# Performance work log

Measured on AMD Instinct MI355X. Metric: run time of the kernel, lower is better.

## Reference

```python
import jax, jax.numpy as jnp
import numpy as np

B, T, W = 4, 2048, 1024
K, G = 7, 8            # kernel_size, groups
Cg = W // G            # channels per group
SE_R = 16              # SE reduction ratio
LN_EPS = 1e-5


def setup_inputs() -> dict:
    key = jax.random.key(0)
    ks = jax.random.split(key, 8)
    h = jax.random.normal(ks[0], (B, T, W), jnp.float32)
    # mask: True = padding; valid prefix of random length per row
    lengths = jax.random.randint(ks[1], (B,), T // 2, T + 1)
    mask = jnp.arange(T)[None, :] >= lengths[:, None]
    s_w = np.float32(1.0 / np.sqrt(W))
    return dict(
        h=h,
        mask=mask,
        offset_w=jax.random.normal(ks[2], (W, K), jnp.float32) * 0.01,
        offset_b=jnp.zeros((K,), jnp.float32),
        conv_w=jax.random.normal(ks[3], (G, Cg, Cg, K), jnp.float32) * np.float32(1.0 / np.sqrt(Cg * K)),
        conv_b=jnp.zeros((W,), jnp.float32),
        ln_g=jnp.ones((W,), jnp.float32),
        ln_b=jnp.zeros((W,), jnp.float32),
        se_w1=jax.random.normal(ks[4], (W, W // SE_R), jnp.float32) * s_w,
        se_b1=jnp.zeros((W // SE_R,), jnp.float32),
        se_w2=jax.random.normal(ks[5], (W // SE_R, W), jnp.float32) * np.float32(1.0 / np.sqrt(W // SE_R)),
        se_b2=jnp.zeros((W,), jnp.float32),
        proj_w=jax.random.normal(ks[6], (W, 1), jnp.float32) * s_w,
        proj_b=jnp.zeros((1,), jnp.float32),
    )


def deform_conv1d(h, offset_w, offset_b, conv_w, conv_b):
    # h: [B,T,W]. Learned per-(position, tap) fractional offsets; linear interp gather;
    # grouped conv combine. conv_w: [G, out_per_group, in_per_group, K].
    Bn, Tn, Wn = h.shape
    pad = (K - 1) // 2
    offsets = h @ offset_w + offset_b                                   # [B,T,K]
    base = (jnp.arange(Tn, dtype=jnp.float32)[None, :, None]
            + (jnp.arange(K, dtype=jnp.float32) - pad)[None, None, :])  # [1,T,K]
    pos = jnp.clip(base + offsets, 0.0, Tn - 1.0)                       # [B,T,K]
    p0 = jnp.floor(pos).astype(jnp.int32)
    p1 = jnp.minimum(p0 + 1, Tn - 1)
    frac = (pos - p0.astype(jnp.float32))[..., None]                    # [B,T,K,1]
    gather = jax.vmap(lambda hb, ib: hb[ib])                            # [T,W],[T,K] -> [T,K,W]
    sampled = gather(h, p0) * (1.0 - frac) + gather(h, p1) * frac       # [B,T,K,W]
    sg = sampled.reshape(Bn, Tn, K, G, Cg)
    out = jnp.einsum('btkgc,gock->btgo', sg, conv_w).reshape(Bn, Tn, Wn)
    return out + conv_b


def layer_norm(x, g, b):
    mu = jnp.mean(x, axis=-1, keepdims=True)
    var = jnp.mean(jnp.square(x - mu), axis=-1, keepdims=True)
    return (x - mu) * jax.lax.rsqrt(var + LN_EPS) * g + b


def se_block(x, mask, w1, b1, w2, b2):
    valid = (~mask).astype(x.dtype)[..., None]                          # [B,T,1]
    lengths = jnp.clip(jnp.sum(valid, axis=1), 1.0)                     # [B,1]
    s = jnp.sum(x * valid, axis=1) / lengths                            # [B,W]
    gate = jax.nn.sigmoid(jax.nn.relu(s @ w1 + b1) @ w2 + b2)           # [B,W]
    return x * gate[:, None, :]


def reference(h, mask, offset_w, offset_b, conv_w, conv_b, ln_g, ln_b,
              se_w1, se_b1, se_w2, se_b2, proj_w, proj_b):
    x = layer_norm(deform_conv1d(h, offset_w, offset_b, conv_w, conv_b), ln_g, ln_b)
    x = se_block(x, mask, se_w1, se_b1, se_w2, se_b2)
    # dropout: identity in eval mode (p handled outside reference)
    valid = (~mask).astype(x.dtype)[..., None]
    x = x * valid                                                       # masked_fill(mask, 0)
    lengths = jnp.clip(jnp.sum(valid, axis=1), 1.0)                     # [B,1]
    pooled = jnp.sum(x, axis=1) / lengths                               # [B,W]
    return jnp.squeeze(pooled @ proj_w + proj_b, axis=-1)               # [B]
```

## Files before the change

### kernel.cpp

```cpp
#include <hip/hip_runtime.h>
#include <hip/hip_bf16.h>

#define Bdim 4
#define Tdim 2048
#define Wdim 1024
#define Kdim 7
#define Gdim 8
#define Cg   128
#define Hdim 64
#define TT   64

typedef __attribute__((ext_vector_type(8))) short short8v;
typedef __attribute__((ext_vector_type(4))) float float4v;

__device__ __forceinline__ short f2bf(float x) {
    union { float f; unsigned u; } v; v.f = x;
    unsigned r = v.u + 0x7fff + ((v.u >> 16) & 1);
    return (short)(r >> 16);
}

__device__ __forceinline__ unsigned pack2bf(float lo, float hi) {
    return __builtin_amdgcn_perm(__float_as_uint(hi) + 0x8000u,
                                 __float_as_uint(lo) + 0x8000u, 0x07060302u);
}

__device__ __forceinline__ short8v lerp_pack(uint4 a, uint4 b, float f) {
    union { uint4 u; short8v s; } r;
    const unsigned* pa = (const unsigned*)&a;
    const unsigned* pb = (const unsigned*)&b;
    unsigned* pr = (unsigned*)&r.u;
#pragma unroll
    for (int d = 0; d < 4; d++) {
        float alo = __uint_as_float(pa[d] << 16);
        float ahi = __uint_as_float(pa[d] & 0xffff0000u);
        float blo = __uint_as_float(pb[d] << 16);
        float bhi = __uint_as_float(pb[d] & 0xffff0000u);
        float rlo = alo + f * (blo - alo);
        float rhi = ahi + f * (bhi - ahi);
        pr[d] = pack2bf(rlo, rhi);
    }
    return r.s;
}

__global__ __launch_bounds__(256) void k_pre(const float* __restrict__ conv_w,
                                             short* __restrict__ Wtb,
                                             const float* __restrict__ h,
                                             const float* __restrict__ offset_w,
                                             const float* __restrict__ offset_b,
                                             float* __restrict__ pos,
                                             ushort* __restrict__ h16,
                                             float* __restrict__ s_sum) {
    int tid = threadIdx.x;
    if (blockIdx.x < 448) {
        if (blockIdx.x == 0) {
#pragma unroll
            for (int i = 0; i < 16; i++) s_sum[tid + i * 256] = 0.f;
        }
        int i = blockIdx.x * 256 + tid;
        int cb = i & 15;
        int o = (i >> 4) & 127;
        int gk = i >> 11;
        int k = gk % Kdim, g = gk / Kdim;
        const float* src = conv_w + ((size_t)(g * Cg + o) * Cg + cb * 8) * Kdim + k;
        short8v pk;
#pragma unroll
        for (int j = 0; j < 8; j++) pk[j] = f2bf(src[(size_t)j * Kdim]);
        short8v* Wtb8 = (short8v*)Wtb;
        Wtb8[(size_t)gk * 2048 + o * 16 + cb] = pk;
        return;
    }
    int lane = tid & 63, wv = tid >> 6;
    int bt = (blockIdx.x - 448) * 4 + wv;
    int t = bt & (Tdim - 1);
    const float* row = h + (size_t)bt * Wdim;
    float acc[Kdim];
#pragma unroll
    for (int k = 0; k < Kdim; k++) acc[k] = 0.f;
#pragma unroll
    for (int j = 0; j < 4; j++) {
        int c = lane * 4 + j * 256;
        float4 hv = *(const float4*)(row + c);
        const float* ow = offset_w + (size_t)c * Kdim;
#pragma unroll
        for (int k = 0; k < Kdim; k++)
            acc[k] += hv.x * ow[k] + hv.y * ow[Kdim + k] + hv.z * ow[2 * Kdim + k]
                    + hv.w * ow[3 * Kdim + k];
        ushort4 hp;
        hp.x = (ushort)f2bf(hv.x); hp.y = (ushort)f2bf(hv.y);
        hp.z = (ushort)f2bf(hv.z); hp.w = (ushort)f2bf(hv.w);
        *(ushort4*)(h16 + (size_t)bt * Wdim + c) = hp;
    }
#pragma unroll
    for (int k = 0; k < Kdim; k++) {
#pragma unroll
        for (int m = 32; m > 0; m >>= 1) acc[k] += __shfl_xor(acc[k], m);
    }
    if (lane < Kdim) {
        float o = acc[lane] + offset_b[lane];
        float base = (float)t + (float)(lane - 3);
        float p = fminf(fmaxf(base + o, 0.f), (float)(Tdim - 1));
        pos[bt * Kdim + lane] = p;
    }
}

__global__ __launch_bounds__(256, 4) void k_conv(const ushort* __restrict__ h16,
                                                 const short* __restrict__ Wtb,
                                                 const float* __restrict__ conv_b,
                                                 const float* __restrict__ pos,
                                                 ushort* __restrict__ y16) {
    __shared__ short8v sA8[2][TT * 16];

    int blk = blockIdx.x;
    int g  = blk & 7;
    int tc = (blk >> 3) & 31;
    int b  = blk >> 8;
    int t0 = tc * TT;
    int tid = threadIdx.x;
    int lane = tid & 63, wv = tid >> 6;
    int r15 = lane & 15, q = lane >> 4;

    const ushort* hb = h16 + (size_t)(b * Tdim) * Wdim + g * Cg;
    const short8v* WtbV = (const short8v*)Wtb + (size_t)(g * Kdim) * 2048;

    int scb = tid & 15;
    int sr0 = tid >> 4;

    float4v acc[4][2];
#pragma unroll
    for (int tt = 0; tt < 4; tt++)
#pragma unroll
        for (int n = 0; n < 2; n++) acc[tt][n] = (float4v){0.f, 0.f, 0.f, 0.f};

#pragma unroll 1
    for (int k = 0; k < Kdim; k++) {
        short8v bfr[8];
#pragma unroll
        for (int n = 0; n < 2; n++)
#pragma unroll
            for (int kk = 0; kk < 4; kk++)
                bfr[n * 4 + kk] =
                    WtbV[(size_t)k * 2048 + (wv * 32 + n * 16 + r15) * 16 + kk * 4 + q];
        short8v* buf = sA8[k & 1];
#pragma unroll
        for (int i = 0; i < 4; i++) {
            int r = sr0 + i * 16;
            float p = pos[(b * Tdim + t0 + r) * Kdim + k];
            int p0 = (int)p;
            float f = p - (float)p0;
            int p1 = min(p0 + 1, Tdim - 1);
            uint4 lo = *(const uint4*)(hb + (size_t)p0 * Wdim + scb * 8);
            uint4 hi = *(const uint4*)(hb + (size_t)p1 * Wdim + scb * 8);
            buf[r * 16 + (scb ^ (r & 7))] = lerp_pack(lo, hi, f);
        }
        __syncthreads();
#pragma unroll
        for (int tt = 0; tt < 4; tt++) {
            int r = tt * 16 + r15;
            short8v af[4];
#pragma unroll
            for (int kk = 0; kk < 4; kk++)
                af[kk] = buf[r * 16 + ((kk * 4 + q) ^ (r & 7))];
#pragma unroll
            for (int kk = 0; kk < 4; kk++) {
#pragma unroll
                for (int n = 0; n < 2; n++)
                    acc[tt][n] = __builtin_amdgcn_mfma_f32_16x16x32_bf16(
                        af[kk], bfr[n * 4 + kk], acc[tt][n], 0, 0, 0);
            }
        }
    }
    __syncthreads();
    float* ep = (float*)sA8;
#pragma unroll
    for (int n = 0; n < 2; n++) {
        int colb = wv * 32 + n * 16 + r15;
        float bias = conv_b[g * Cg + colb];
#pragma unroll
        for (int tt = 0; tt < 4; tt++)
#pragma unroll
            for (int j = 0; j < 4; j++) {
                int row = tt * 16 + q * 4 + j;
                ep[row * 128 + (colb ^ ((row & 7) << 2))] = acc[tt][n][j] + bias;
            }
    }
    __syncthreads();
    int row = tid >> 2, c0 = (tid & 3) * 32;
    int sw = (row & 7) << 2;
    ushort* yp = y16 + (size_t)(b * Tdim + t0 + row) * Wdim + g * Cg + c0;
#pragma unroll
    for (int s = 0; s < 4; s++) {
        float4 va = *(const float4*)&ep[row * 128 + ((c0 + s * 8) ^ sw)];
        float4 vb = *(const float4*)&ep[row * 128 + ((c0 + s * 8 + 4) ^ sw)];
        uint4 o;
        o.x = pack2bf(va.x, va.y);
        o.y = pack2bf(va.z, va.w);
        o.z = pack2bf(vb.x, vb.y);
        o.w = pack2bf(vb.z, vb.w);
        *(uint4*)(yp + s * 8) = o;
    }
}

__global__ __launch_bounds__(256) void k_lnpool(const ushort* __restrict__ y16,
                                                const int* __restrict__ mask,
                                                float* __restrict__ s_sum) {
    int blk = blockIdx.x;
    int b = blk >> 6, ch = blk & 63;
    int tid = threadIdx.x;
    int lane = tid & 63, wv = tid >> 6;
    __shared__ float red[4 * Wdim];

    float accv[2][8];
#pragma unroll
    for (int j = 0; j < 2; j++)
#pragma unroll
        for (int e = 0; e < 8; e++) accv[j][e] = 0.f;

    for (int i = 0; i < 8; i++) {
        int t = ch * 32 + wv * 8 + i;
        if (mask[b * Tdim + t]) continue;
        const ushort* yr = y16 + (size_t)(b * Tdim + t) * Wdim;
        float v[2][8];
        float s = 0.f, qq = 0.f;
#pragma unroll
        for (int j = 0; j < 2; j++) {
            uint4 u = *(const uint4*)(yr + lane * 8 + j * 512);
            const unsigned* pu = (const unsigned*)&u;
#pragma unroll
            for (int d = 0; d < 4; d++) {
                float lo = __uint_as_float(pu[d] << 16);
                float hi = __uint_as_float(pu[d] & 0xffff0000u);
                v[j][d * 2] = lo; v[j][d * 2 + 1] = hi;
                s += lo + hi; qq += lo * lo + hi * hi;
            }
        }
#pragma unroll
        for (int m = 32; m > 0; m >>= 1) { s += __shfl_xor(s, m); qq += __shfl_xor(qq, m); }
        float mu = s * (1.f / Wdim);
        float inv = rsqrtf(qq * (1.f / Wdim) - mu * mu + 1e-5f);
#pragma unroll
        for (int j = 0; j < 2; j++)
#pragma unroll
            for (int e = 0; e < 8; e++) accv[j][e] += (v[j][e] - mu) * inv;
    }
#pragma unroll
    for (int j = 0; j < 2; j++) {
        *(float4*)(&red[wv * Wdim + lane * 8 + j * 512]) =
            (float4){accv[j][0], accv[j][1], accv[j][2], accv[j][3]};
        *(float4*)(&red[wv * Wdim + lane * 8 + j * 512 + 4]) =
            (float4){accv[j][4], accv[j][5], accv[j][6], accv[j][7]};
    }
    __syncthreads();
#pragma unroll
    for (int e = 0; e < 4; e++) {
        int w = tid + e * 256;
        float a = red[w] + red[Wdim + w] + red[2 * Wdim + w] + red[3 * Wdim + w];
        atomicAdd(&s_sum[b * Wdim + w], a);
    }
}

__global__ __launch_bounds__(256) void k_sefinal(const float* __restrict__ s_sum,
                                                 const int* __restrict__ mask,
                                                 const float* __restrict__ ln_g,
                                                 const float* __restrict__ ln_b,
                                                 const float* __restrict__ w1,
                                                 const float* __restrict__ b1,
                                                 const float* __restrict__ w2,
                                                 const float* __restrict__ b2,
                                                 const float* __restrict__ projw,
                                                 const float* __restrict__ projb,
                                                 float* __restrict__ out) {
    int b = blockIdx.x, tid = threadIdx.x;
    __shared__ float s[Wdim];
    __shared__ float hred[4][Hdim];
    __shared__ float hid[Hdim];
    __shared__ float rbuf[4];
    __shared__ float sLinv;
    int lane = tid & 63, wv = tid >> 6;

    int cnt = 0;
    for (int t = tid; t < Tdim; t += 256) cnt += (mask[b * Tdim + t] ? 0 : 1);
    float fc = (float)cnt;
#pragma unroll
    for (int off = 32; off > 0; off >>= 1) fc += __shfl_down(fc, off);
    if (lane == 0) rbuf[wv] = fc;
    __syncthreads();
    if (tid == 0) {
        float L = rbuf[0] + rbuf[1] + rbuf[2] + rbuf[3];
        sLinv = 1.f / fmaxf(L, 1.f);
    }
    __syncthreads();
    float Linv = sLinv;

    int w4 = tid * 4;
    float4 a = *(const float4*)(s_sum + b * Wdim + w4);
    float4 gg = *(const float4*)(ln_g + w4);
    float4 bb = *(const float4*)(ln_b + w4);
    s[w4 + 0] = gg.x * (a.x * Linv) + bb.x;
    s[w4 + 1] = gg.y * (a.y * Linv) + bb.y;
    s[w4 + 2] = gg.z * (a.z * Linv) + bb.z;
    s[w4 + 3] = gg.w * (a.w * Linv) + bb.w;
    __syncthreads();

    int j = tid & 63, p = tid >> 6;
    float ha = 0.f;
    for (int w = p * 256; w < (p + 1) * 256; ++w) ha += s[w] * w1[(size_t)w * Hdim + j];
    hred[p][j] = ha;
    __syncthreads();
    if (tid < Hdim)
        hid[tid] = fmaxf(hred[0][tid] + hred[1][tid] + hred[2][tid] + hred[3][tid] + b1[tid], 0.f);
    __syncthreads();

    float part = 0.f;
    for (int w = tid; w < Wdim; w += 256) {
        float ga = b2[w];
#pragma unroll 8
        for (int j2 = 0; j2 < Hdim; j2++) ga += hid[j2] * w2[(size_t)j2 * Wdim + w];
        float gate = 1.f / (1.f + expf(-ga));
        part += s[w] * gate * projw[w];
    }
#pragma unroll
    for (int off = 32; off > 0; off >>= 1) part += __shfl_down(part, off);
    __syncthreads();
    if (lane == 0) rbuf[wv] = part;
    __syncthreads();
    if (tid == 0) out[b] = rbuf[0] + rbuf[1] + rbuf[2] + rbuf[3] + projb[0];
}

extern "C" void kernel_launch(void* const* d_in, const int* in_sizes, int n_in,
                              void* d_out, int out_size, void* d_ws, size_t ws_size,
                              hipStream_t stream) {
    const float* h        = (const float*)d_in[0];
    const int*   mask     = (const int*)d_in[1];
    const float* offset_w = (const float*)d_in[2];
    const float* offset_b = (const float*)d_in[3];
    const float* conv_w   = (const float*)d_in[4];
    const float* conv_b   = (const float*)d_in[5];
    const float* ln_g     = (const float*)d_in[6];
    const float* ln_b     = (const float*)d_in[7];
    const float* se_w1    = (const float*)d_in[8];
    const float* se_b1    = (const float*)d_in[9];
    const float* se_w2    = (const float*)d_in[10];
    const float* se_b2    = (const float*)d_in[11];
    const float* proj_w   = (const float*)d_in[12];
    const float* proj_b   = (const float*)d_in[13];
    float* out = (float*)d_out;

    char* wsb = (char*)d_ws;
    float*  pos   = (float*)(wsb);
    ushort* h16   = (ushort*)(wsb + 229376);
    short*  Wtb   = (short*)(wsb + 17006592);
    ushort* y16   = (ushort*)(wsb + 18841600);
    float*  s_sum = (float*)(wsb + 35618816);

    k_pre<<<dim3(448 + Bdim * Tdim / 4), dim3(256), 0, stream>>>(conv_w, Wtb, h, offset_w,
                                                                 offset_b, pos, h16, s_sum);
    k_conv<<<dim3(Bdim * (Tdim / TT) * Gdim), dim3(256), 0, stream>>>(h16, Wtb, conv_b,
                                                                      pos, y16);
    k_lnpool<<<dim3(Bdim * 64), dim3(256), 0, stream>>>(y16, mask, s_sum);
    k_sefinal<<<dim3(Bdim), dim3(256), 0, stream>>>(s_sum, mask, ln_g, ln_b,
                                                    se_w1, se_b1, se_w2, se_b2,
                                                    proj_w, proj_b, out);
}
```

Measured before the change: 99.05 us.

## Prefetch next-tap gathers, stage pos in LDS, fuse LN row stats into conv epilogue

The conv kernel now stages its positions in shared memory and prefetches the h16 gather rows for tap k+1 while the MFMAs for tap k run, hiding gather latency. The conv epilogue computes per-row sum and sum of squares in fp32 and adds them atomically into a new rowstat buffer, which k_pre zeroes. k_lnpool then reads those stats instead of reducing each row itself, and its shared-memory reduction is replaced by a simpler per-thread column accumulation. This adds extra global atomics and registers in the conv kernel, and statistics now come from fp32 values rather than the bf16-rounded ones.

```diff
diff --git a/kernel.cpp b/kernel.cpp
--- a/kernel.cpp
+++ b/kernel.cpp
@@ -49,13 +49,15 @@
                                              const float* __restrict__ offset_b,
                                              float* __restrict__ pos,
                                              ushort* __restrict__ h16,
-                                             float* __restrict__ s_sum) {
+                                             float* __restrict__ s_sum,
+                                             float* __restrict__ rowstat) {
     int tid = threadIdx.x;
     if (blockIdx.x < 448) {
         if (blockIdx.x == 0) {
 #pragma unroll
             for (int i = 0; i < 16; i++) s_sum[tid + i * 256] = 0.f;
         }
+        if (blockIdx.x < 64) rowstat[blockIdx.x * 256 + tid] = 0.f;
         int i = blockIdx.x * 256 + tid;
         int cb = i & 15;
         int o = (i >> 4) & 127;
@@ -107,8 +109,10 @@
                                                  const short* __restrict__ Wtb,
                                                  const float* __restrict__ conv_b,
                                                  const float* __restrict__ pos,
-                                                 ushort* __restrict__ y16) {
+                                                 ushort* __restrict__ y16,
+                                                 float* __restrict__ rowstat) {
     __shared__ short8v sA8[2][TT * 16];
+    __shared__ float posl[TT * 8];
 
     int blk = blockIdx.x;
     int g  = blk & 7;
@@ -125,11 +129,33 @@
     int scb = tid & 15;
     int sr0 = tid >> 4;
 
+    {
+        int base = (b * Tdim + t0) * Kdim;
+        for (int u = tid; u < TT * Kdim; u += 256) {
+            int r = u / 7, kk = u - r * 7;
+            posl[r * 8 + kk] = pos[base + u];
+        }
+    }
+    __syncthreads();
+
     float4v acc[4][2];
 #pragma unroll
     for (int tt = 0; tt < 4; tt++)
 #pragma unroll
         for (int n = 0; n < 2; n++) acc[tt][n] = (float4v){0.f, 0.f, 0.f, 0.f};
+
+    float fr[4];
+    uint4 glo[4], ghi[4];
+#pragma unroll
+    for (int i = 0; i < 4; i++) {
+        int r = sr0 + i * 16;
+        float p = posl[r * 8 + 0];
+        int p0 = (int)p;
+        fr[i] = p - (float)p0;
+        int p1 = min(p0 + 1, Tdim - 1);
+        glo[i] = *(const uint4*)(hb + (size_t)p0 * Wdim + scb * 8);
+        ghi[i] = *(const uint4*)(hb + (size_t)p1 * Wdim + scb * 8);
+    }
 
 #pragma unroll 1
     for (int k = 0; k < Kdim; k++) {
@@ -144,15 +170,21 @@
 #pragma unroll
         for (int i = 0; i < 4; i++) {
             int r = sr0 + i * 16;
-            float p = pos[(b * Tdim + t0 + r) * Kdim + k];
-            int p0 = (int)p;
-            float f = p - (float)p0;
-            int p1 = min(p0 + 1, Tdim - 1);
-            uint4 lo = *(const uint4*)(hb + (size_t)p0 * Wdim + scb * 8);
-            uint4 hi = *(const uint4*)(hb + (size_t)p1 * Wdim + scb * 8);
-            buf[r * 16 + (scb ^ (r & 7))] = lerp_pack(lo, hi, f);
+            buf[r * 16 + (scb ^ (r & 7))] = lerp_pack(glo[i], ghi[i], fr[i]);
         }
         __syncthreads();
+        if (k < Kdim - 1) {
+#pragma unroll
+            for (int i = 0; i < 4; i++) {
+                int r = sr0 + i * 16;
+                float p = posl[r * 8 + k + 1];
+                int p0 = (int)p;
+                fr[i] = p - (float)p0;
+                int p1 = min(p0 + 1, Tdim - 1);
+                glo[i] = *(const uint4*)(hb + (size_t)p0 * Wdim + scb * 8);
+                ghi[i] = *(const uint4*)(hb + (size_t)p1 * Wdim + scb * 8);
+            }
+        }
 #pragma unroll
         for (int tt = 0; tt < 4; tt++) {
             int r = tt * 16 + r15;
@@ -187,10 +219,14 @@
     int row = tid >> 2, c0 = (tid & 3) * 32;
     int sw = (row & 7) << 2;
     ushort* yp = y16 + (size_t)(b * Tdim + t0 + row) * Wdim + g * Cg + c0;
+    float s_part = 0.f, q_part = 0.f;
 #pragma unroll
     for (int s = 0; s < 4; s++) {
         float4 va = *(const float4*)&ep[row * 128 + ((c0 + s * 8) ^ sw)];
         float4 vb = *(const float4*)&ep[row * 128 + ((c0 + s * 8 + 4) ^ sw)];
+        s_part += va.x + va.y + va.z + va.w + vb.x + vb.y + vb.z + vb.w;
+        q_part += va.x * va.x + va.y * va.y + va.z * va.z + va.w * va.w
+                + vb.x * vb.x + vb.y * vb.y + vb.z * vb.z + vb.w * vb.w;
         uint4 o;
         o.x = pack2bf(va.x, va.y);
         o.y = pack2bf(va.z, va.w);
@@ -198,64 +234,42 @@
         o.w = pack2bf(vb.z, vb.w);
         *(uint4*)(yp + s * 8) = o;
     }
+    s_part += __shfl_xor(s_part, 1); s_part += __shfl_xor(s_part, 2);
+    q_part += __shfl_xor(q_part, 1); q_part += __shfl_xor(q_part, 2);
+    if ((tid & 3) == 0) {
+        atomicAdd(&rowstat[(b * Tdim + t0 + row) * 2 + 0], s_part);
+        atomicAdd(&rowstat[(b * Tdim + t0 + row) * 2 + 1], q_part);
+    }
 }
 
 __global__ __launch_bounds__(256) void k_lnpool(const ushort* __restrict__ y16,
                                                 const int* __restrict__ mask,
+                                                const float* __restrict__ rowstat,
                                                 float* __restrict__ s_sum) {
     int blk = blockIdx.x;
     int b = blk >> 6, ch = blk & 63;
     int tid = threadIdx.x;
-    int lane = tid & 63, wv = tid >> 6;
-    __shared__ float red[4 * Wdim];
-
-    float accv[2][8];
-#pragma unroll
-    for (int j = 0; j < 2; j++)
-#pragma unroll
-        for (int e = 0; e < 8; e++) accv[j][e] = 0.f;
-
-    for (int i = 0; i < 8; i++) {
-        int t = ch * 32 + wv * 8 + i;
+    int c0 = tid * 4;
+    float a0 = 0.f, a1 = 0.f, a2 = 0.f, a3 = 0.f;
+    for (int i = 0; i < 32; i++) {
+        int t = ch * 32 + i;
         if (mask[b * Tdim + t]) continue;
-        const ushort* yr = y16 + (size_t)(b * Tdim + t) * Wdim;
-        float v[2][8];
-        float s = 0.f, qq = 0.f;
-#pragma unroll
-        for (int j = 0; j < 2; j++) {
-            uint4 u = *(const uint4*)(yr + lane * 8 + j * 512);
-            const unsigned* pu = (const unsigned*)&u;
-#pragma unroll
-            for (int d = 0; d < 4; d++) {
-                float lo = __uint_as_float(pu[d] << 16);
-                float hi = __uint_as_float(pu[d] & 0xffff0000u);
-                v[j][d * 2] = lo; v[j][d * 2 + 1] = hi;
-                s += lo + hi; qq += lo * lo + hi * hi;
-            }
-        }
-#pragma unroll
-        for (int m = 32; m > 0; m >>= 1) { s += __shfl_xor(s, m); qq += __shfl_xor(qq, m); }
-        float mu = s * (1.f / Wdim);
-        float inv = rsqrtf(qq * (1.f / Wdim) - mu * mu + 1e-5f);
-#pragma unroll
-        for (int j = 0; j < 2; j++)
-#pragma unroll
-            for (int e = 0; e < 8; e++) accv[j][e] += (v[j][e] - mu) * inv;
-    }
-#pragma unroll
-    for (int j = 0; j < 2; j++) {
-        *(float4*)(&red[wv * Wdim + lane * 8 + j * 512]) =
-            (float4){accv[j][0], accv[j][1], accv[j][2], accv[j][3]};
-        *(float4*)(&red[wv * Wdim + lane * 8 + j * 512 + 4]) =
-            (float4){accv[j][4], accv[j][5], accv[j][6], accv[j][7]};
-    }
-    __syncthreads();
-#pragma unroll
-    for (int e = 0; e < 4; e++) {
-        int w = tid + e * 256;
-        float a = red[w] + red[Wdim + w] + red[2 * Wdim + w] + red[3 * Wdim + w];
-        atomicAdd(&s_sum[b * Wdim + w], a);
-    }
+        float st = rowstat[(b * Tdim + t) * 2 + 0];
+        float sq = rowstat[(b * Tdim + t) * 2 + 1];
+        float mu = st * (1.f / Wdim);
+        float inv = rsqrtf(sq * (1.f / Wdim) - mu * mu + 1e-5f);
+        uint2 u = *(const uint2*)(y16 + (size_t)(b * Tdim + t) * Wdim + c0);
+        float v0 = __uint_as_float(u.x << 16);
+        float v1 = __uint_as_float(u.x & 0xffff0000u);
+        float v2 = __uint_as_float(u.y << 16);
+        float v3 = __uint_as_float(u.y & 0xffff0000u);
+        a0 += (v0 - mu) * inv; a1 += (v1 - mu) * inv;
+        a2 += (v2 - mu) * inv; a3 += (v3 - mu) * inv;
+    }
+    atomicAdd(&s_sum[b * Wdim + c0 + 0], a0);
+    atomicAdd(&s_sum[b * Wdim + c0 + 1], a1);
+    atomicAdd(&s_sum[b * Wdim + c0 + 2], a2);
+    atomicAdd(&s_sum[b * Wdim + c0 + 3], a3);
 }
 
 __global__ __launch_bounds__(256) void k_sefinal(const float* __restrict__ s_sum,
@@ -346,17 +360,19 @@
     float* out = (float*)d_out;
 
     char* wsb = (char*)d_ws;
-    float*  pos   = (float*)(wsb);
-    ushort* h16   = (ushort*)(wsb + 229376);
-    short*  Wtb   = (short*)(wsb + 17006592);
-    ushort* y16   = (ushort*)(wsb + 18841600);
-    float*  s_sum = (float*)(wsb + 35618816);
+    float*  pos     = (float*)(wsb);
+    ushort* h16     = (ushort*)(wsb + 229376);
+    short*  Wtb     = (short*)(wsb + 17006592);
+    ushort* y16     = (ushort*)(wsb + 18841600);
+    float*  s_sum   = (float*)(wsb + 35618816);
+    float*  rowstat = (float*)(wsb + 35635200);
 
     k_pre<<<dim3(448 + Bdim * Tdim / 4), dim3(256), 0, stream>>>(conv_w, Wtb, h, offset_w,
-                                                                 offset_b, pos, h16, s_sum);
+                                                                 offset_b, pos, h16, s_sum,
+                                                                 rowstat);
     k_conv<<<dim3(Bdim * (Tdim / TT) * Gdim), dim3(256), 0, stream>>>(h16, Wtb, conv_b,
-                                                                      pos, y16);
-    k_lnpool<<<dim3(Bdim * 64), dim3(256), 0, stream>>>(y16, mask, s_sum);
+                                                                      pos, y16, rowstat);
+    k_lnpool<<<dim3(Bdim * 64), dim3(256), 0, stream>>>(y16, mask, rowstat, s_sum);
     k_sefinal<<<dim3(Bdim), dim3(256), 0, stream>>>(s_sum, mask, ln_g, ln_b,
                                                     se_w1, se_b1, se_w2, se_b2,
                                                     proj_w, proj_b, out);
```

Result: slower. 106.6 us (+7.6%).
